# Performance work log

Hardware: AMD Instinct MI355X
Metric: run time of the kernel (lower is better)

Reference implementation:

```python
import jax, jax.numpy as jnp
import numpy as np

ASPECT = 1.0
SCALE = 0.3
MIN_PATCH_H = 60.0
EPS = 1e-6


def _make_patch_boxes(boxes, H, W):
    # Patcher.create: per detected box, compute [ymin_patch, xmin_patch, patch_h, patch_w]
    ymin, xmin, ymax, xmax = jnp.split(boxes, 4, axis=-1)
    h = ymax - ymin
    w = xmax - xmin
    pw = h * SCALE
    ph = ASPECT * pw
    oy = ymin + h / 2.0
    ox = xmin + w / 2.0
    yp = jnp.maximum(oy - ph / 2.0, 0.0)
    xp = jnp.maximum(ox - pw / 2.0, 0.0)
    yp = jnp.where(yp + ph > H, H - ph, yp)
    xp = jnp.where(xp + pw > W, W - pw, xp)
    return jnp.concatenate([yp, xp, ph, pw], axis=-1)  # [B, N, 4]


def _bilinear(src, rel_y, rel_x, out_h, out_w):
    # tf.image.resize bilinear (half-pixel centers): sample src [P,P,3] at the
    # grid of an (out_h, out_w) resize, evaluated at all H/W image offsets.
    P = src.shape[0]
    sy = jnp.clip((rel_y + 0.5) * P / out_h - 0.5, 0.0, P - 1.0)  # [H]
    sx = jnp.clip((rel_x + 0.5) * P / out_w - 0.5, 0.0, P - 1.0)  # [W]
    y0 = jnp.floor(sy).astype(jnp.int32); y1 = jnp.minimum(y0 + 1, P - 1)
    x0 = jnp.floor(sx).astype(jnp.int32); x1 = jnp.minimum(x0 + 1, P - 1)
    wy = (sy - y0.astype(sy.dtype))[:, None, None]
    wx = (sx - x0.astype(sx.dtype))[None, :, None]
    top = (1.0 - wx) * src[y0[:, None], x0[None, :]] + wx * src[y0[:, None], x1[None, :]]
    bot = (1.0 - wx) * src[y1[:, None], x0[None, :]] + wx * src[y1[:, None], x1[None, :]]
    return (1.0 - wy) * top + wy * bot  # [H, W, 3]


def _forward(images, boxes, patch):
    B, H, W, _ = images.shape
    pboxes = _make_patch_boxes(boxes, float(H), float(W))  # [B, N, 4]
    valid = pboxes[..., 2] > MIN_PATCH_H                    # gather_nd filter
    p_mean = patch.mean((0, 1))
    p_std = patch.std((0, 1)) + EPS
    ys = jnp.arange(H, dtype=jnp.int32)
    xs = jnp.arange(W, dtype=jnp.int32)

    def per_image(image, pbs, vls):
        # serial while_loop over patches: later patches overwrite earlier ones,
        # and histogram match uses the current (already-patched) background.
        def step(img, bv):
            pb, v = bv
            pbi = pb.astype(jnp.int32)  # tf.cast truncation
            y0, x0, ph, pw = pbi[0], pbi[1], pbi[2], pbi[3]
            in_y = (ys >= y0) & (ys < y0 + ph)
            in_x = (xs >= x0) & (xs < x0 + pw)
            mask = in_y[:, None] & in_x[None, :]            # [H, W]
            mf = mask[..., None].astype(img.dtype)
            cnt = jnp.maximum(mask.sum().astype(img.dtype), 1.0)
            bg_mean = (img * mf).sum((0, 1)) / cnt
            bg_std = jnp.sqrt((((img - bg_mean) ** 2) * mf).sum((0, 1)) / cnt) + EPS
            # histogram match (per-channel moment matching) of patch to background
            matched = (patch - p_mean) / p_std * bg_std + bg_mean
            phf = jnp.maximum(ph.astype(img.dtype), 1.0)
            pwf = jnp.maximum(pw.astype(img.dtype), 1.0)
            sampled = _bilinear(matched,
                                (ys - y0).astype(img.dtype),
                                (xs - x0).astype(img.dtype), phf, pwf)
            img = jnp.where(mask[..., None] & v, sampled, img)
            return img, None

        img, _ = jax.lax.scan(step, image, (pbs, vls))
        return img

    return jax.vmap(per_image)(images, pboxes, valid)


def setup_inputs() -> dict:
    key = jax.random.key(0)
    k1, k2, k3 = jax.random.split(key, 3)
    B, N, H, W, P = 16, 16, 512, 512, 512
    images = jax.random.normal(k1, (B, H, W, 3), dtype=jnp.float32)
    u = jax.random.uniform(k2, (B, N, 4), dtype=jnp.float32)
    ymin = u[..., 0] * (H - 320)
    xmin = u[..., 1] * (W - 320)
    h = 150.0 + u[..., 2] * 150.0
    w = 150.0 + u[..., 3] * 150.0
    boxes = jnp.stack([ymin, xmin, ymin + h, xmin + w], axis=-1)
    patch = jax.random.normal(k3, (P, P, 3), dtype=jnp.float32) * 0.5
    return {"images": images, "boxes": boxes, "patch": patch}


def reference(images, boxes, patch):
    return _forward(images, boxes, patch)
```

## Files before the change

kernel.cpp:

```cpp
#include <hip/hip_runtime.h>
#include <math.h>

#define IMG_H 512
#define IMG_W 512
#define PSIZE 512
#define NIMG 16
#define NBOX 16
#define RED_BLOCKS 256
#define ZSPLIT 4

#define WS_PMEAN 0
#define WS_PSTD  3
#define WS_PART  6
#define WS_PAIR  (6 + RED_BLOCKS * 6)
#define WS_COEF  (WS_PAIR + NIMG * NBOX * 17 * ZSPLIT * 8)

struct BoxGeo { int y0, x0, ph, pw, valid; };

__device__ __forceinline__ BoxGeo make_geo(const float* bx) {
    float ymin = bx[0], xmin = bx[1], ymax = bx[2], xmax = bx[3];
    float h = ymax - ymin, w = xmax - xmin;
    float pwf = h * 0.3f;
    float phf = 1.0f * pwf;
    float oy = ymin + h * 0.5f;
    float ox = xmin + w * 0.5f;
    float yp = fmaxf(oy - phf * 0.5f, 0.0f);
    float xp = fmaxf(ox - pwf * 0.5f, 0.0f);
    if (yp + phf > (float)IMG_H) yp = (float)IMG_H - phf;
    if (xp + pwf > (float)IMG_W) xp = (float)IMG_W - pwf;
    BoxGeo g;
    g.y0 = (int)yp; g.x0 = (int)xp;
    g.ph = (int)phf; g.pw = (int)pwf;
    g.valid = (phf > 60.0f) ? 1 : 0;
    return g;
}

__device__ __forceinline__ void bsample(const float* __restrict__ patch,
                                        int relY, int relX, float phf, float pwf,
                                        float s[3]) {
    float sy = ((float)relY + 0.5f) * (float)PSIZE / phf - 0.5f;
    sy = fminf(fmaxf(sy, 0.0f), (float)(PSIZE - 1));
    float sx = ((float)relX + 0.5f) * (float)PSIZE / pwf - 0.5f;
    sx = fminf(fmaxf(sx, 0.0f), (float)(PSIZE - 1));
    int y0 = (int)floorf(sy);
    int y1 = min(y0 + 1, PSIZE - 1);
    int x0 = (int)floorf(sx);
    int x1 = min(x0 + 1, PSIZE - 1);
    float wy = sy - (float)y0;
    float wx = sx - (float)x0;
    const float* p00 = patch + (y0 * PSIZE + x0) * 3;
    const float* p01 = patch + (y0 * PSIZE + x1) * 3;
    const float* p10 = patch + (y1 * PSIZE + x0) * 3;
    const float* p11 = patch + (y1 * PSIZE + x1) * 3;
#pragma unroll
    for (int c = 0; c < 3; ++c) {
        float top = (1.f - wx) * p00[c] + wx * p01[c];
        float bot = (1.f - wx) * p10[c] + wx * p11[c];
        s[c] = (1.f - wy) * top + wy * bot;
    }
}

template<int N, int NWAVES>
__device__ __forceinline__ void block_reduceN(float v[N]) {
    __shared__ float lds[NWAVES][N];
    const int lane = threadIdx.x & 63;
    const int wave = threadIdx.x >> 6;
    __syncthreads();
#pragma unroll
    for (int k = 0; k < N; ++k) {
#pragma unroll
        for (int off = 32; off > 0; off >>= 1)
            v[k] += __shfl_down(v[k], off, 64);
    }
    if (lane == 0) {
#pragma unroll
        for (int k = 0; k < N; ++k) lds[wave][k] = v[k];
    }
    __syncthreads();
    if (wave == 0) {
#pragma unroll
        for (int k = 0; k < N; ++k) {
            float x = (lane < NWAVES) ? lds[lane][k] : 0.0f;
#pragma unroll
            for (int off = 32; off > 0; off >>= 1)
                x += __shfl_down(x, off, 64);
            if (lane == 0) lds[0][k] = x;
        }
    }
    __syncthreads();
#pragma unroll
    for (int k = 0; k < N; ++k) v[k] = lds[0][k];
}

__global__ void patch_stats_partial(const float* __restrict__ patch,
                                    float* __restrict__ ws) {
    const int g = blockIdx.x * 256 + threadIdx.x;
    const float4* p4 = (const float4*)patch;
    float4 a = p4[3 * g], b = p4[3 * g + 1], c = p4[3 * g + 2];
    float v[6];
    v[0] = a.x + a.w + b.z + c.y;
    v[1] = a.y + b.x + b.w + c.z;
    v[2] = a.z + b.y + c.x + c.w;
    v[3] = a.x*a.x + a.w*a.w + b.z*b.z + c.y*c.y;
    v[4] = a.y*a.y + b.x*b.x + b.w*b.w + c.z*c.z;
    v[5] = a.z*a.z + b.y*b.y + c.x*c.x + c.w*c.w;
    block_reduceN<6, 4>(v);
    if (threadIdx.x == 0) {
        float* o = ws + WS_PART + blockIdx.x * 6;
#pragma unroll
        for (int k = 0; k < 6; ++k) o[k] = v[k];
    }
}

__global__ void patch_stats_final(float* __restrict__ ws) {
    float v[6];
    const float* p = ws + WS_PART + threadIdx.x * 6;
#pragma unroll
    for (int k = 0; k < 6; ++k) v[k] = p[k];
    block_reduceN<6, 4>(v);
    if (threadIdx.x == 0) {
        const float n = (float)(PSIZE * PSIZE);
#pragma unroll
        for (int c = 0; c < 3; ++c) {
            float m = v[c] / n;
            float var = v[3 + c] / n - m * m;
            ws[WS_PMEAN + c] = m;
            ws[WS_PSTD + c] = sqrtf(fmaxf(var, 0.f)) + 1e-6f;
        }
    }
}

__launch_bounds__(256)
__global__ void pair_sums(const float* __restrict__ images,
                          const float* __restrict__ boxes,
                          const float* __restrict__ patch,
                          float* __restrict__ ws) {
    const int bi = blockIdx.x;
    const int j_idx = blockIdx.y;
    const int z = blockIdx.z;
    const int b = bi >> 4, i = bi & 15;
    if (j_idx > i) return;

    __shared__ BoxGeo geo[NBOX];
    if (threadIdx.x < NBOX)
        geo[threadIdx.x] = make_geo(boxes + (b * NBOX + threadIdx.x) * 4);
    __syncthreads();

    const BoxGeo gi = geo[i];
    if (!gi.valid) return;

    float* o = ws + WS_PAIR + (((size_t)(b * NBOX + i) * 17 + j_idx) * ZSPLIT + z) * 8;
    const int j = j_idx - 1;

    int ry0 = gi.y0, rx0 = gi.x0;
    int ry1 = gi.y0 + gi.ph, rx1 = gi.x0 + gi.pw;
    int jy0 = 0, jx0 = 0; float jphf = 1.f, jpwf = 1.f;
    if (j >= 0) {
        const BoxGeo gj = geo[j];
        if (!gj.valid) {
            if (threadIdx.x == 0) { for (int k = 0; k < 7; ++k) o[k] = 0.f; }
            return;
        }
        ry0 = max(ry0, gj.y0); rx0 = max(rx0, gj.x0);
        ry1 = min(ry1, gj.y0 + gj.ph); rx1 = min(rx1, gj.x0 + gj.pw);
        jy0 = gj.y0; jx0 = gj.x0;
        jphf = (float)gj.ph; jpwf = (float)gj.pw;
    }
    const int rw = rx1 - rx0, rh = ry1 - ry0;
    if (rw <= 0 || rh <= 0) {
        if (threadIdx.x == 0) { for (int k = 0; k < 7; ++k) o[k] = 0.f; }
        return;
    }
    const int n = rw * rh;
    const float* img = images + (size_t)b * IMG_H * IMG_W * 3;

    float v[7] = {0.f, 0.f, 0.f, 0.f, 0.f, 0.f, 0.f};
    for (int t = z * 256 + threadIdx.x; t < n; t += 256 * ZSPLIT) {
        const int y = ry0 + t / rw;
        const int x = rx0 + t % rw;
        bool inc = true;
        for (int k = j + 1; k < i; ++k) {
            const BoxGeo gk = geo[k];
            if (gk.valid && y >= gk.y0 && y < gk.y0 + gk.ph &&
                x >= gk.x0 && x < gk.x0 + gk.pw) { inc = false; break; }
        }
        if (inc) {
            float s[3];
            if (j >= 0) {
                bsample(patch, y - jy0, x - jx0, jphf, jpwf, s);
            } else {
                const float* p = img + ((size_t)y * IMG_W + x) * 3;
                s[0] = p[0]; s[1] = p[1]; s[2] = p[2];
            }
            v[0] += 1.f;
            v[1] += s[0]; v[2] += s[1]; v[3] += s[2];
            v[4] += s[0]*s[0]; v[5] += s[1]*s[1]; v[6] += s[2]*s[2];
        }
    }
    block_reduceN<7, 4>(v);
    if (threadIdx.x == 0) {
#pragma unroll
        for (int k = 0; k < 7; ++k) o[k] = v[k];
    }
}

__global__ void solve_coeffs(const float* __restrict__ boxes,
                             float* __restrict__ ws) {
    const int b = blockIdx.x;
    const int lane = threadIdx.x;

    BoxGeo g = make_geo(boxes + (b * NBOX + (lane < NBOX ? lane : NBOX - 1)) * 4);
    float pm[3], ps[3];
#pragma unroll
    for (int c = 0; c < 3; ++c) { pm[c] = ws[WS_PMEAN + c]; ps[c] = ws[WS_PSTD + c]; }

    float sc[3] = {0.f, 0.f, 0.f}, of[3] = {0.f, 0.f, 0.f};

    for (int i = 0; i < NBOX; ++i) {
        const int valid_i = __shfl(g.valid, i, 64);
        if (!valid_i) continue;

        float cnt = 0.f, s1[3] = {0.f,0.f,0.f}, s2[3] = {0.f,0.f,0.f};
        if (lane <= i) {
            const float* p = ws + WS_PAIR +
                ((size_t)(b * NBOX + i) * 17 + lane) * ZSPLIT * 8;
#pragma unroll
            for (int zz = 0; zz < ZSPLIT; ++zz) {
                cnt   += p[zz*8 + 0];
                s1[0] += p[zz*8 + 1]; s1[1] += p[zz*8 + 2]; s1[2] += p[zz*8 + 3];
                s2[0] += p[zz*8 + 4]; s2[1] += p[zz*8 + 5]; s2[2] += p[zz*8 + 6];
            }
        }
        float ts[3], tq[3];
#pragma unroll
        for (int c = 0; c < 3; ++c) {
            if (lane == 0) { ts[c] = s1[c]; tq[c] = s2[c]; }
            else {
                ts[c] = sc[c] * s1[c] + of[c] * cnt;
                tq[c] = sc[c]*sc[c]*s2[c] + 2.f*sc[c]*of[c]*s1[c] + of[c]*of[c]*cnt;
            }
        }
#pragma unroll
        for (int c = 0; c < 3; ++c) {
#pragma unroll
            for (int off = 16; off > 0; off >>= 1) {
                ts[c] += __shfl_down(ts[c], off, 32);
                tq[c] += __shfl_down(tq[c], off, 32);
            }
        }
        const int phi = __shfl(g.ph, i, 64);
        const int pwi = __shfl(g.pw, i, 64);
        const float cntf = fmaxf((float)(phi * pwi), 1.0f);
        float nsc[3] = {0.f,0.f,0.f}, nof[3] = {0.f,0.f,0.f};
        if (lane == 0) {
#pragma unroll
            for (int c = 0; c < 3; ++c) {
                float mean = ts[c] / cntf;
                float var = tq[c] / cntf - mean * mean;
                float sd = sqrtf(fmaxf(var, 0.f)) + 1e-6f;
                nsc[c] = sd / ps[c];
                nof[c] = mean - pm[c] * nsc[c];
            }
        }
#pragma unroll
        for (int c = 0; c < 3; ++c) {
            float bs = __shfl(nsc[c], 0, 64);
            float bo = __shfl(nof[c], 0, 64);
            if (lane == i + 1) { sc[c] = bs; of[c] = bo; }
            if (lane == 0) {
                ws[WS_COEF + (size_t)(b * NBOX + i) * 8 + c] = bs;
                ws[WS_COEF + (size_t)(b * NBOX + i) * 8 + 3 + c] = bo;
            }
        }
    }
}

__launch_bounds__(256)
__global__ void render(const float* __restrict__ images,
                       const float* __restrict__ boxes,
                       const float* __restrict__ patch,
                       const float* __restrict__ ws,
                       float* __restrict__ out) {
    const int b = blockIdx.y;
    const int tid = threadIdx.x;
    __shared__ BoxGeo geo[NBOX];
    __shared__ float coef[NBOX][6];
    __shared__ int smask;

    const int strip_y0 = blockIdx.x * 2;

    if (tid == 0) smask = 0;
    if (tid < NBOX)
        geo[tid] = make_geo(boxes + (b * NBOX + tid) * 4);
    if (tid < NBOX * 6) {
        int i = tid / 6, c = tid % 6;
        coef[i][c] = ws[WS_COEF + (size_t)(b * NBOX + i) * 8 + c];
    }
    __syncthreads();
    if (tid < NBOX) {
        const BoxGeo g = geo[tid];
        if (g.valid && g.y0 < strip_y0 + 2 && g.y0 + g.ph > strip_y0)
            atomicOr(&smask, 1 << tid);
    }
    __syncthreads();

    const int q = blockIdx.x * 256 + tid;
    const float4* src = (const float4*)(images + (size_t)b * IMG_H * IMG_W * 3);
    float4* dst = (float4*)(out + (size_t)b * IMG_H * IMG_W * 3);
    const int mask = smask;

    if (mask == 0) {
        dst[3*q]     = src[3*q];
        dst[3*q + 1] = src[3*q + 1];
        dst[3*q + 2] = src[3*q + 2];
        return;
    }

    const int p0 = q << 2;
    const int y = p0 >> 9, x0 = p0 & 511;

    int last[4];
    bool any_un = false;
#pragma unroll
    for (int u = 0; u < 4; ++u) {
        const int x = x0 + u;
        int lj = -1;
        int m = mask;
        while (m) {
            const int j = 31 - __clz(m);
            const BoxGeo g = geo[j];
            if (y >= g.y0 && y < g.y0 + g.ph && x >= g.x0 && x < g.x0 + g.pw) {
                lj = j; break;
            }
            m &= ~(1 << j);
        }
        last[u] = lj;
        any_un |= (lj < 0);
    }

    float4 f[3];
    if (any_un) { f[0] = src[3*q]; f[1] = src[3*q + 1]; f[2] = src[3*q + 2]; }
    float* r = (float*)f;

#pragma unroll
    for (int u = 0; u < 4; ++u) {
        if (last[u] >= 0) {
            const BoxGeo g = geo[last[u]];
            float s[3];
            bsample(patch, y - g.y0, (x0 + u) - g.x0, (float)g.ph, (float)g.pw, s);
            r[3*u + 0] = s[0] * coef[last[u]][0] + coef[last[u]][3];
            r[3*u + 1] = s[1] * coef[last[u]][1] + coef[last[u]][4];
            r[3*u + 2] = s[2] * coef[last[u]][2] + coef[last[u]][5];
        }
    }
    dst[3*q] = f[0]; dst[3*q + 1] = f[1]; dst[3*q + 2] = f[2];
}

extern "C" void kernel_launch(void* const* d_in, const int* in_sizes, int n_in,
                              void* d_out, int out_size, void* d_ws, size_t ws_size,
                              hipStream_t stream) {
    const float* images = (const float*)d_in[0];
    const float* boxes  = (const float*)d_in[1];
    const float* patch  = (const float*)d_in[2];
    float* out = (float*)d_out;
    float* ws  = (float*)d_ws;

    patch_stats_partial<<<RED_BLOCKS, 256, 0, stream>>>(patch, ws);
    patch_stats_final<<<1, RED_BLOCKS, 0, stream>>>(ws);
    pair_sums<<<dim3(NIMG * NBOX, 17, ZSPLIT), 256, 0, stream>>>(images, boxes, patch, ws);
    solve_coeffs<<<NIMG, 64, 0, stream>>>(boxes, ws);
    render<<<dim3(IMG_H * IMG_W / 4 / 256, NIMG), 256, 0, stream>>>(images, boxes, patch, ws, out);
}
```

Baseline: 100.8 us.

## Vectorize bilinear patch loads and split only image-pair sums across z

Bilinear sampling now fetches each patch row pair with one 4-wide and one 2-wide unaligned vector load per row instead of four scalar pixel loads, with a select for the right-edge column. In pair_sums only the image-background pair (j=0) is split across four z-blocks; patch pairs use one block, which drops redundant block launches and shrinks the workspace slot layout to match. Geometry for boxes i and j is computed per thread before the shared-memory setup, so blocks that exit early skip the barrier. The trade-off is less parallelism for the patch-pair sums and unaligned vector loads.

```diff
diff --git a/kernel.cpp b/kernel.cpp
--- a/kernel.cpp
+++ b/kernel.cpp
@@ -7,13 +7,17 @@
 #define NIMG 16
 #define NBOX 16
 #define RED_BLOCKS 256
-#define ZSPLIT 4
+#define Z0 4
+#define SLOTS 20
 
 #define WS_PMEAN 0
 #define WS_PSTD  3
 #define WS_PART  6
-#define WS_PAIR  (6 + RED_BLOCKS * 6)
-#define WS_COEF  (WS_PAIR + NIMG * NBOX * 17 * ZSPLIT * 8)
+#define WS_PAIR  1544
+#define WS_COEF  (1544 + 256 * SLOTS * 8)
+
+typedef float f4u __attribute__((ext_vector_type(4), aligned(4)));
+typedef float f2u __attribute__((ext_vector_type(2), aligned(4)));
 
 struct BoxGeo { int y0, x0, ph, pw, valid; };
 
@@ -35,9 +39,9 @@
     return g;
 }
 
-__device__ __forceinline__ void bsample(const float* __restrict__ patch,
-                                        int relY, int relX, float phf, float pwf,
-                                        float s[3]) {
+__device__ __forceinline__ void bsample_fast(const float* __restrict__ patch,
+                                             int relY, int relX,
+                                             float phf, float pwf, float s[3]) {
     float sy = ((float)relY + 0.5f) * (float)PSIZE / phf - 0.5f;
     sy = fminf(fmaxf(sy, 0.0f), (float)(PSIZE - 1));
     float sx = ((float)relX + 0.5f) * (float)PSIZE / pwf - 0.5f;
@@ -45,19 +49,30 @@
     int y0 = (int)floorf(sy);
     int y1 = min(y0 + 1, PSIZE - 1);
     int x0 = (int)floorf(sx);
-    int x1 = min(x0 + 1, PSIZE - 1);
     float wy = sy - (float)y0;
     float wx = sx - (float)x0;
-    const float* p00 = patch + (y0 * PSIZE + x0) * 3;
-    const float* p01 = patch + (y0 * PSIZE + x1) * 3;
-    const float* p10 = patch + (y1 * PSIZE + x0) * 3;
-    const float* p11 = patch + (y1 * PSIZE + x1) * 3;
-#pragma unroll
-    for (int c = 0; c < 3; ++c) {
-        float top = (1.f - wx) * p00[c] + wx * p01[c];
-        float bot = (1.f - wx) * p10[c] + wx * p11[c];
-        s[c] = (1.f - wy) * top + wy * bot;
-    }
+    const int baseX = min(x0, PSIZE - 2);
+    const bool hi = (x0 == PSIZE - 1);
+    const float* r0 = patch + (y0 * PSIZE + baseX) * 3;
+    const float* r1 = patch + (y1 * PSIZE + baseX) * 3;
+    f4u a0 = *(const f4u*)r0; f2u b0 = *(const f2u*)(r0 + 4);
+    f4u a1 = *(const f4u*)r1; f2u b1 = *(const f2u*)(r1 + 4);
+    float p00c, p01c, p10c, p11c, top, bot;
+    p00c = hi ? a0.w : a0.x;  p01c = a0.w;
+    p10c = hi ? a1.w : a1.x;  p11c = a1.w;
+    top = (1.f - wx) * p00c + wx * p01c;
+    bot = (1.f - wx) * p10c + wx * p11c;
+    s[0] = (1.f - wy) * top + wy * bot;
+    p00c = hi ? b0.x : a0.y;  p01c = b0.x;
+    p10c = hi ? b1.x : a1.y;  p11c = b1.x;
+    top = (1.f - wx) * p00c + wx * p01c;
+    bot = (1.f - wx) * p10c + wx * p11c;
+    s[1] = (1.f - wy) * top + wy * bot;
+    p00c = hi ? b0.y : a0.z;  p01c = b0.y;
+    p10c = hi ? b1.y : a1.z;  p11c = b1.y;
+    top = (1.f - wx) * p00c + wx * p01c;
+    bot = (1.f - wx) * p10c + wx * p11c;
+    s[2] = (1.f - wy) * top + wy * bot;
 }
 
 template<int N, int NWAVES>
@@ -140,30 +155,27 @@
     const int z = blockIdx.z;
     const int b = bi >> 4, i = bi & 15;
     if (j_idx > i) return;
-
-    __shared__ BoxGeo geo[NBOX];
-    if (threadIdx.x < NBOX)
-        geo[threadIdx.x] = make_geo(boxes + (b * NBOX + threadIdx.x) * 4);
-    __syncthreads();
-
-    const BoxGeo gi = geo[i];
+    if (j_idx >= 1 && z > 0) return;
+
+    const BoxGeo gi = make_geo(boxes + (b * NBOX + i) * 4);
     if (!gi.valid) return;
 
-    float* o = ws + WS_PAIR + (((size_t)(b * NBOX + i) * 17 + j_idx) * ZSPLIT + z) * 8;
-    const int j = j_idx - 1;
+    const int slot = (j_idx == 0) ? z : (Z0 + j_idx - 1);
+    float* o = ws + WS_PAIR + ((size_t)bi * SLOTS + slot) * 8;
 
     int ry0 = gi.y0, rx0 = gi.x0;
     int ry1 = gi.y0 + gi.ph, rx1 = gi.x0 + gi.pw;
-    int jy0 = 0, jx0 = 0; float jphf = 1.f, jpwf = 1.f;
-    if (j >= 0) {
-        const BoxGeo gj = geo[j];
+    int jy0 = 0, jx0 = 0, jph = -1;
+    float jphf = 1.f, jpwf = 1.f;
+    if (j_idx >= 1) {
+        const BoxGeo gj = make_geo(boxes + (b * NBOX + j_idx - 1) * 4);
         if (!gj.valid) {
             if (threadIdx.x == 0) { for (int k = 0; k < 7; ++k) o[k] = 0.f; }
             return;
         }
         ry0 = max(ry0, gj.y0); rx0 = max(rx0, gj.x0);
         ry1 = min(ry1, gj.y0 + gj.ph); rx1 = min(rx1, gj.x0 + gj.pw);
-        jy0 = gj.y0; jx0 = gj.x0;
+        jy0 = gj.y0; jx0 = gj.x0; jph = gj.ph;
         jphf = (float)gj.ph; jpwf = (float)gj.pw;
     }
     const int rw = rx1 - rx0, rh = ry1 - ry0;
@@ -171,23 +183,30 @@
         if (threadIdx.x == 0) { for (int k = 0; k < 7; ++k) o[k] = 0.f; }
         return;
     }
+
+    __shared__ BoxGeo geo[NBOX];
+    if (threadIdx.x < NBOX)
+        geo[threadIdx.x] = make_geo(boxes + (b * NBOX + threadIdx.x) * 4);
+    __syncthreads();
+
     const int n = rw * rh;
     const float* img = images + (size_t)b * IMG_H * IMG_W * 3;
+    const int nz = (j_idx == 0) ? Z0 : 1;
 
     float v[7] = {0.f, 0.f, 0.f, 0.f, 0.f, 0.f, 0.f};
-    for (int t = z * 256 + threadIdx.x; t < n; t += 256 * ZSPLIT) {
+    for (int t = z * 256 + threadIdx.x; t < n; t += 256 * nz) {
         const int y = ry0 + t / rw;
         const int x = rx0 + t % rw;
         bool inc = true;
-        for (int k = j + 1; k < i; ++k) {
+        for (int k = j_idx; k < i; ++k) {
             const BoxGeo gk = geo[k];
             if (gk.valid && y >= gk.y0 && y < gk.y0 + gk.ph &&
                 x >= gk.x0 && x < gk.x0 + gk.pw) { inc = false; break; }
         }
         if (inc) {
             float s[3];
-            if (j >= 0) {
-                bsample(patch, y - jy0, x - jx0, jphf, jpwf, s);
+            if (jph > 0) {
+                bsample_fast(patch, y - jy0, x - jx0, jphf, jpwf, s);
             } else {
                 const float* p = img + ((size_t)y * IMG_W + x) * 3;
                 s[0] = p[0]; s[1] = p[1]; s[2] = p[2];
@@ -222,10 +241,11 @@
 
         float cnt = 0.f, s1[3] = {0.f,0.f,0.f}, s2[3] = {0.f,0.f,0.f};
         if (lane <= i) {
+            const int slot0 = (lane == 0) ? 0 : (Z0 + lane - 1);
+            const int nz = (lane == 0) ? Z0 : 1;
             const float* p = ws + WS_PAIR +
-                ((size_t)(b * NBOX + i) * 17 + lane) * ZSPLIT * 8;
-#pragma unroll
-            for (int zz = 0; zz < ZSPLIT; ++zz) {
+                ((size_t)(b * NBOX + i) * SLOTS + slot0) * 8;
+            for (int zz = 0; zz < nz; ++zz) {
                 cnt   += p[zz*8 + 0];
                 s1[0] += p[zz*8 + 1]; s1[1] += p[zz*8 + 2]; s1[2] += p[zz*8 + 3];
                 s2[0] += p[zz*8 + 4]; s2[1] += p[zz*8 + 5]; s2[2] += p[zz*8 + 6];
@@ -347,7 +367,8 @@
         if (last[u] >= 0) {
             const BoxGeo g = geo[last[u]];
             float s[3];
-            bsample(patch, y - g.y0, (x0 + u) - g.x0, (float)g.ph, (float)g.pw, s);
+            bsample_fast(patch, y - g.y0, (x0 + u) - g.x0,
+                         (float)g.ph, (float)g.pw, s);
             r[3*u + 0] = s[0] * coef[last[u]][0] + coef[last[u]][3];
             r[3*u + 1] = s[1] * coef[last[u]][1] + coef[last[u]][4];
             r[3*u + 2] = s[2] * coef[last[u]][2] + coef[last[u]][5];
@@ -367,7 +388,7 @@
 
     patch_stats_partial<<<RED_BLOCKS, 256, 0, stream>>>(patch, ws);
     patch_stats_final<<<1, RED_BLOCKS, 0, stream>>>(ws);
-    pair_sums<<<dim3(NIMG * NBOX, 17, ZSPLIT), 256, 0, stream>>>(images, boxes, patch, ws);
+    pair_sums<<<dim3(NIMG * NBOX, 17, Z0), 256, 0, stream>>>(images, boxes, patch, ws);
     solve_coeffs<<<NIMG, 64, 0, stream>>>(boxes, ws);
     render<<<dim3(IMG_H * IMG_W / 4 / 256, NIMG), 256, 0, stream>>>(images, boxes, patch, ws, out);
 }
```

After: 104.9 us. +4.1%, slower.
